# Kernel optimization log

Measured on AMD Instinct MI355X. Metric: run time of the kernel, lower is better.

The kernel has to match this reference:

```python
import jax, jax.numpy as jnp
import numpy as np

B, N, DIM = 32, 1025, 768
H, D = 12, 64
THETA = 100.0


def setup_inputs() -> dict:
    key = jax.random.key(0)
    k0, k1, k2, k3 = jax.random.split(key, 4)
    x = jax.random.normal(k0, (B, N, DIM), dtype=jnp.float32)
    W_qkv = jax.random.normal(k1, (3 * H * D, DIM), dtype=jnp.float32) * 0.02
    W_out = jax.random.normal(k2, (DIM, H * D), dtype=jnp.float32) * 0.02
    b_out = jnp.zeros((DIM,), dtype=jnp.float32)
    # performer random projection buffer: randn(num_features, dim_head) * sqrt(2/dim_head)
    projection = jax.random.normal(k3, (D, D), dtype=jnp.float32) * np.sqrt(2.0 / D)
    # RoPE frequencies for content tokens (n-1 positions, dim_head/2 pairs)
    inv_freq = 1.0 / (THETA ** (np.arange(0, D, 2, dtype=np.float32) / D))  # (D/2,)
    t = np.arange(N - 1, dtype=np.float32)
    angles = np.outer(t, inv_freq)  # (N-1, D/2)
    freqs_cos = jnp.asarray(np.cos(angles), dtype=jnp.float32)
    freqs_sin = jnp.asarray(np.sin(angles), dtype=jnp.float32)
    return {"x": x, "W_qkv": W_qkv, "W_out": W_out, "b_out": b_out,
            "projection": projection, "freqs_cos": freqs_cos, "freqs_sin": freqs_sin}


def reference(x, W_qkv, W_out, b_out, projection, freqs_cos, freqs_sin):
    b, n, _ = x.shape
    h, d = H, D
    # qkv projection and split: 'b n (qkv h d) -> qkv b h n d'
    qkv = jnp.einsum('bnf,gf->bng', x, W_qkv).reshape(b, n, 3, h, d)
    q = jnp.transpose(qkv[:, :, 0], (0, 2, 1, 3))  # (b,h,n,d)
    k = jnp.transpose(qkv[:, :, 1], (0, 2, 1, 3))
    v = jnp.transpose(qkv[:, :, 2], (0, 2, 1, 3))

    def rope(t):
        # rotate content tokens (skip CLS token 0); complex mult as real math
        tc = t[:, :, 1:].reshape(b, h, n - 1, d // 2, 2)
        ev, od = tc[..., 0], tc[..., 1]
        c = freqs_cos[None, None]
        s = freqs_sin[None, None]
        rot = jnp.stack([ev * c - od * s, ev * s + od * c], axis=-1).reshape(b, h, n - 1, d)
        return jnp.concatenate([t[:, :, :1], rot], axis=2)

    q = rope(q)
    k = rope(k)

    def feature_map(t):
        # x * d^{-1/4}, project with (feat, d), relu + eps
        tp = jnp.einsum('bhnd,jd->bhnj', t * (d ** -0.25), projection)
        return jax.nn.relu(tp) + 1e-6

    qf = feature_map(q)
    kf = feature_map(k)

    # non-causal linear attention
    k_sum = kf.sum(axis=-2)                              # (b,h,j)
    context = jnp.einsum('bhnd,bhne->bhde', kf, v)       # (b,h,feat,d)
    D_inv = 1.0 / jnp.einsum('bhnd,bhd->bhn', qf, k_sum)
    out = jnp.einsum('bhde,bhnd,bhn->bhne', context, qf, D_inv)  # (b,h,n,d)

    out = jnp.transpose(out, (0, 2, 1, 3)).reshape(b, n, h * d)
    return jnp.einsum('bnf,gf->bng', out, W_out) + b_out
```

## Files before the change

### kernel.cpp

```cpp
#include <hip/hip_runtime.h>
#include <stdint.h>
#include <stddef.h>

typedef __bf16 bft;
typedef __bf16 bf16x4 __attribute__((ext_vector_type(4)));
typedef __bf16 bf16x8 __attribute__((ext_vector_type(8)));
typedef float f32x4 __attribute__((ext_vector_type(4)));

#define NH 12
#define HD 64
#define SEQ 1025
#define NB 32
#define DMODEL 768
#define MROWS (NB * SEQ)
#define BHN (NB * NH)
#define BSTR 1040
#define MP (NB * BSTR)
#define SEQP 1056

__device__ __forceinline__ void gl_lds16(const void* g, void* l) {
  __builtin_amdgcn_global_load_lds(
      (const __attribute__((address_space(1))) void*)g,
      (__attribute__((address_space(3))) void*)l, 16, 0, 0);
}

__device__ __forceinline__ bf16x4 ds_tr16(const bft* p, int boff) {
  bf16x4 d;
  asm volatile("ds_read_b64_tr_b16 %0, %1 offset:%2"
               : "=v"(d)
               : "v"((const __attribute__((address_space(3))) bft*)p), "i"(boff)
               : "memory");
  return d;
}

__device__ __forceinline__ void lgkm0() {
  asm volatile("s_waitcnt lgkmcnt(0)" ::: "memory");
}

__global__ __launch_bounds__(256) void k_cast(
    const float* __restrict__ S, bft* __restrict__ D, int n4) {
  int i = blockIdx.x * 256 + threadIdx.x;
  if (i < n4) {
    f32x4 v = *(const f32x4*)(S + (size_t)i * 4);
    bf16x4 o;
    o[0] = (bft)v[0]; o[1] = (bft)v[1]; o[2] = (bft)v[2]; o[3] = (bft)v[3];
    *(bf16x4*)(D + (size_t)i * 4) = o;
  }
}

__global__ __launch_bounds__(256) void k_padzero(bft* __restrict__ KFT, bft* __restrict__ VT) {
  int r = blockIdx.x * 256 + threadIdx.x;
  if (r < BHN * 64) {
    bft* a = KFT + (size_t)r * SEQP + 1025;
    bft* b = VT + (size_t)r * SEQP + 1025;
#pragma unroll
    for (int i = 0; i < 31; ++i) { a[i] = (bft)0.f; b[i] = (bft)0.f; }
  }
}

__global__ __launch_bounds__(256) void k_qkv_gemm(
    const bft* __restrict__ X, const bft* __restrict__ W,
    const bft* __restrict__ P,
    const float* __restrict__ FC, const float* __restrict__ FS,
    bft* __restrict__ QF, bft* __restrict__ KFT, bft* __restrict__ VT) {
  __shared__ __align__(16) bft sA[128 * 64];
  __shared__ __align__(16) bft sB[128 * 64];
  __shared__ __align__(16) bft sP[64 * 64];
  const int tid = threadIdx.x;
  const int lane = tid & 63;
  const int lm = lane & 15;
  const int quad = lane >> 4;
  const int wid = tid >> 6;
  const int wm = (wid & 1) << 6;
  const int wn = (wid >> 1) << 6;
  const int m0 = blockIdx.x * 128;
  const int n0 = blockIdx.y * 128;
  const int sw = lm & 7;
  const int o0 = (quad ^ sw) << 3;
  const int o1 = ((4 + quad) ^ sw) << 3;

#pragma unroll
  for (int it = 0; it < 2; it++) {
    int c = it * 256 + tid;
    int row = c >> 3;
    int col = ((c & 7) ^ (row & 7)) << 3;
    gl_lds16(P + row * 64 + col, sP + c * 8);
  }

  f32x4 acc[4][4] = {};

  for (int kt = 0; kt < DMODEL; kt += 64) {
#pragma unroll
    for (int it = 0; it < 4; it++) {
      int c = it * 256 + tid;
      int row = c >> 3;
      int col = ((c & 7) ^ (row & 7)) << 3;
      int ar = m0 + row;
      int b2 = ar / BSTR;
      int nn = ar - b2 * BSTR;
      if (nn > 1024) nn = 1024;
      gl_lds16(X + (size_t)(b2 * SEQ + nn) * DMODEL + kt + col, sA + c * 8);
      gl_lds16(W + (size_t)(n0 + row) * DMODEL + kt + col, sB + c * 8);
    }
    __syncthreads();
#pragma unroll
    for (int kk = 0; kk < 2; kk++) {
      const int off = kk ? o1 : o0;
      bf16x8 af[4], bb[4];
#pragma unroll
      for (int i = 0; i < 4; i++)
        af[i] = *(const bf16x8*)(sA + (wm + i * 16 + lm) * 64 + off);
#pragma unroll
      for (int j = 0; j < 4; j++)
        bb[j] = *(const bf16x8*)(sB + (wn + j * 16 + lm) * 64 + off);
#pragma unroll
      for (int i = 0; i < 4; i++)
#pragma unroll
        for (int j = 0; j < 4; j++)
          acc[i][j] = __builtin_amdgcn_mfma_f32_16x16x32_bf16(af[i], bb[j], acc[i][j], 0, 0, 0);
    }
    __syncthreads();
  }

  const int s = blockIdx.y / 6;
  const int h = ((n0 + wn) - s * DMODEL) >> 6;

  bft* tt = sA + wid * 1024;
  const bft* tl = tt + quad * 128 + lm * 4;

  if (s < 2) {
#pragma unroll
    for (int i = 0; i < 4; i++) {
      const int tbase = m0 + wm + i * 16;
      const int bb2 = tbase / BSTR;
      const int nb = tbase - bb2 * BSTR;
#pragma unroll
      for (int j = 0; j < 4; j++) {
        const int d = j * 16 + lm;
        const int fj = d >> 1;
        bf16x4 w;
#pragma unroll
        for (int r = 0; r < 4; r++) {
          float v = acc[i][j][r];
          float pv = __shfl_xor(v, 1);
          int n = nb + quad * 4 + r;
          float ov = v;
          if (n >= 1) {
            int nc = (n <= 1024) ? n : 1024;
            float cc = FC[(nc - 1) * 32 + fj];
            float ss = FS[(nc - 1) * 32 + fj];
            ov = (d & 1) ? (pv * ss + v * cc) : (v * cc - pv * ss);
          }
          w[r] = (bft)ov;
        }
        *(bf16x4*)(tt + d * 16 + quad * 4) = w;
      }
      lgkm0();
      bf16x4 i0a = ds_tr16(tl, 0);
      bf16x4 i0b = ds_tr16(tl, 128);
      bf16x4 i1a = ds_tr16(tl, 1024);
      bf16x4 i1b = ds_tr16(tl, 1152);
      lgkm0();
      __builtin_amdgcn_sched_barrier(0);
      bf16x8 af0, af1;
#pragma unroll
      for (int e = 0; e < 4; e++) {
        af0[e] = i0a[e]; af0[e + 4] = i0b[e];
        af1[e] = i1a[e]; af1[e + 4] = i1b[e];
      }

      if (s == 0) {
        const int n = nb + lm;
        const bool valid = (n < SEQ);
        bft* dst = QF + ((size_t)(bb2 * NH + h) * SEQ + n) * HD;
#pragma unroll
        for (int j2 = 0; j2 < 4; j2++) {
          bf16x8 p0 = *(const bf16x8*)(sP + (j2 * 16 + lm) * 64 + o0);
          bf16x8 p1 = *(const bf16x8*)(sP + (j2 * 16 + lm) * 64 + o1);
          f32x4 fa = {0.f, 0.f, 0.f, 0.f};
          fa = __builtin_amdgcn_mfma_f32_16x16x32_bf16(p0, af0, fa, 0, 0, 0);
          fa = __builtin_amdgcn_mfma_f32_16x16x32_bf16(p1, af1, fa, 0, 0, 0);
          bf16x4 o;
#pragma unroll
          for (int r = 0; r < 4; r++) {
            float v = fa[r] * 0.35355339f;
            o[r] = (bft)(fmaxf(v, 0.f) + 1e-6f);
          }
          if (valid) *(bf16x4*)(dst + j2 * 16 + quad * 4) = o;
        }
      } else {
        const int nq = nb + quad * 4;
#pragma unroll
        for (int j2 = 0; j2 < 4; j2++) {
          bf16x8 p0 = *(const bf16x8*)(sP + (j2 * 16 + lm) * 64 + o0);
          bf16x8 p1 = *(const bf16x8*)(sP + (j2 * 16 + lm) * 64 + o1);
          f32x4 fa = {0.f, 0.f, 0.f, 0.f};
          fa = __builtin_amdgcn_mfma_f32_16x16x32_bf16(af0, p0, fa, 0, 0, 0);
          fa = __builtin_amdgcn_mfma_f32_16x16x32_bf16(af1, p1, fa, 0, 0, 0);
          bf16x4 o;
#pragma unroll
          for (int r = 0; r < 4; r++) {
            float v = fa[r] * 0.35355339f;
            o[r] = (bft)(fmaxf(v, 0.f) + 1e-6f);
          }
          bft* rowp = KFT + ((size_t)(bb2 * NH + h) * 64 + j2 * 16 + lm) * SEQP;
          if (nq + 3 <= 1024) {
            *(bf16x4*)(rowp + nq) = o;
          } else {
#pragma unroll
            for (int r = 0; r < 4; r++)
              if (nq + r <= 1024) rowp[nq + r] = o[r];
          }
        }
      }
    }
  } else {
#pragma unroll
    for (int i = 0; i < 4; i++) {
      const int tbase = m0 + wm + i * 16;
      const int bb2 = tbase / BSTR;
      const int nb = tbase - bb2 * BSTR;
      const int nq = nb + quad * 4;
#pragma unroll
      for (int j = 0; j < 4; j++) {
        bf16x4 o;
#pragma unroll
        for (int r = 0; r < 4; r++) o[r] = (bft)acc[i][j][r];
        bft* rowp = VT + ((size_t)(bb2 * NH + h) * 64 + j * 16 + lm) * SEQP;
        if (nq + 3 <= 1024) {
          *(bf16x4*)(rowp + nq) = o;
        } else {
#pragma unroll
          for (int r = 0; r < 4; r++)
            if (nq + r <= 1024) rowp[nq + r] = o[r];
        }
      }
    }
  }
}

__global__ __launch_bounds__(256) void k_context(
    const bft* __restrict__ KFT, const bft* __restrict__ VT,
    float* __restrict__ CTX, float* __restrict__ KSUM) {
  __shared__ __align__(16) bft sK[64 * 32];
  __shared__ __align__(16) bft sV[64 * 32];
  const int tid = threadIdx.x;
  const int lane = tid & 63;
  const int lm = lane & 15;
  const int quad = lane >> 4;
  const int wid = tid >> 6;
  const int bh = blockIdx.x;
  const int y = blockIdx.y;
  const int c0 = (33 * y) / 4;
  const int c1 = (33 * (y + 1)) / 4;
  const bft* kb = KFT + (size_t)bh * 64 * SEQP;
  const bft* vb = VT + (size_t)bh * 64 * SEQP;
  const int f0 = wid * 16;
  const int srow = tid >> 2;
  const int sch = (tid & 3) * 8;

  bf16x8 ones;
#pragma unroll
  for (int e = 0; e < 8; e++) ones[e] = (bft)1.0f;

  f32x4 acc[4] = {};
  f32x4 ak = {0.f, 0.f, 0.f, 0.f};

  for (int c = c0; c < c1; ++c) {
    const int t0 = c * 32;
    gl_lds16(kb + (size_t)srow * SEQP + t0 + sch, sK + tid * 8);
    gl_lds16(vb + (size_t)srow * SEQP + t0 + sch, sV + tid * 8);
    __syncthreads();
    bf16x8 a = *(const bf16x8*)(sK + (f0 + lm) * 32 + quad * 8);
    ak = __builtin_amdgcn_mfma_f32_16x16x32_bf16(a, ones, ak, 0, 0, 0);
#pragma unroll
    for (int j = 0; j < 4; j++) {
      bf16x8 b = *(const bf16x8*)(sV + (j * 16 + lm) * 32 + quad * 8);
      acc[j] = __builtin_amdgcn_mfma_f32_16x16x32_bf16(a, b, acc[j], 0, 0, 0);
    }
    __syncthreads();
  }

  float* cp = CTX + (size_t)bh * 4096;
#pragma unroll
  for (int j = 0; j < 4; j++)
#pragma unroll
    for (int r = 0; r < 4; r++)
      atomicAdd(&cp[(f0 + quad * 4 + r) * 64 + j * 16 + lm], acc[j][r]);
  if (lm == 0) {
#pragma unroll
    for (int r = 0; r < 4; r++)
      atomicAdd(&KSUM[bh * 64 + f0 + quad * 4 + r], ak[r]);
  }
}

__global__ __launch_bounds__(256) void k_ctxprep(
    const float* __restrict__ CTX, const float* __restrict__ KSUM,
    bft* __restrict__ CTH, bft* __restrict__ CTL,
    bft* __restrict__ KTH, bft* __restrict__ KTL) {
  const int bh = blockIdx.x;
  const int tid = threadIdx.x;
  const int e = tid >> 2;
  const int g = tid & 3;
  const float* src = CTX + (size_t)bh * 4096 + e;
  bf16x8 h0, l0, h1, l1;
#pragma unroll
  for (int k = 0; k < 16; ++k) {
    float v = src[(g * 16 + k) * 64];
    bft hi = (bft)v;
    bft lo = (bft)(v - (float)hi);
    if (k < 8) { h0[k] = hi; l0[k] = lo; }
    else       { h1[k - 8] = hi; l1[k - 8] = lo; }
  }
  const int c0 = (2 * g) ^ (e & 7);
  const int c1 = (2 * g + 1) ^ (e & 7);
  bft* dh = CTH + (size_t)bh * 4096 + e * 64;
  bft* dl = CTL + (size_t)bh * 4096 + e * 64;
  *(bf16x8*)(dh + c0 * 8) = h0;
  *(bf16x8*)(dh + c1 * 8) = h1;
  *(bf16x8*)(dl + c0 * 8) = l0;
  *(bf16x8*)(dl + c1 * 8) = l1;
  if (tid < 64) {
    float v = KSUM[bh * 64 + tid];
    bft hi = (bft)v;
    KTH[bh * 64 + tid] = hi;
    KTL[bh * 64 + tid] = (bft)(v - (float)hi);
  }
}

__global__ __launch_bounds__(256) void k_qside(
    const bft* __restrict__ QF, const bft* __restrict__ CTH,
    const bft* __restrict__ CTL, const bft* __restrict__ KTH,
    const bft* __restrict__ KTL, bft* __restrict__ ATTN) {
  __shared__ __align__(16) bft sq[128 * 64];
  __shared__ __align__(16) bft sh[64 * 64];
  __shared__ __align__(16) bft sl[64 * 64];
  const int tid = threadIdx.x;
  const int lane = tid & 63;
  const int lm = lane & 15;
  const int quad = lane >> 4;
  const int wid = tid >> 6;
  const int bh = blockIdx.x;
  const int n0 = blockIdx.y * 128;
  const bft* qf = QF + ((size_t)bh * SEQ + n0) * HD;

#pragma unroll
  for (int it = 0; it < 4; it++) {
    int c = it * 256 + tid;
    int row = c >> 3;
    int col = ((c & 7) ^ (row & 7)) << 3;
    gl_lds16(qf + (size_t)row * 64 + col, sq + c * 8);
  }
#pragma unroll
  for (int it = 0; it < 2; it++) {
    int c = it * 256 + tid;
    gl_lds16(CTH + (size_t)bh * 4096 + c * 8, sh + c * 8);
    gl_lds16(CTL + (size_t)bh * 4096 + c * 8, sl + c * 8);
  }
  bf16x8 kh0 = *(const bf16x8*)(KTH + bh * 64 + quad * 8);
  bf16x8 kh1 = *(const bf16x8*)(KTH + bh * 64 + 32 + quad * 8);
  bf16x8 kl0 = *(const bf16x8*)(KTL + bh * 64 + quad * 8);
  bf16x8 kl1 = *(const bf16x8*)(KTL + bh * 64 + 32 + quad * 8);
  bf16x8 zz = {};
  bf16x8 ad0 = (lm == 0) ? kh0 : (lm == 1) ? kl0 : zz;
  bf16x8 ad1 = (lm == 0) ? kh1 : (lm == 1) ? kl1 : zz;
  __syncthreads();

  bf16x8 ah[4][2], al[4][2];
#pragma unroll
  for (int eb = 0; eb < 4; eb++)
#pragma unroll
    for (int kc = 0; kc < 2; kc++) {
      const int off = ((quad + 4 * kc) ^ (lm & 7)) * 8;
      ah[eb][kc] = *(const bf16x8*)(sh + (eb * 16 + lm) * 64 + off);
      al[eb][kc] = *(const bf16x8*)(sl + (eb * 16 + lm) * 64 + off);
    }

  const int b = bh / NH;
  const int h = bh - b * NH;
#pragma unroll
  for (int tb2 = 0; tb2 < 2; tb2++) {
    const int tok0 = (wid * 2 + tb2) * 16;
    const int roff = (tok0 + lm) * 64;
    bf16x8 bq0 = *(const bf16x8*)(sq + roff + ((quad) ^ (lm & 7)) * 8);
    bf16x8 bq1 = *(const bf16x8*)(sq + roff + ((4 + quad) ^ (lm & 7)) * 8);
    f32x4 dacc = {0.f, 0.f, 0.f, 0.f};
    dacc = __builtin_amdgcn_mfma_f32_16x16x32_bf16(ad0, bq0, dacc, 0, 0, 0);
    dacc = __builtin_amdgcn_mfma_f32_16x16x32_bf16(ad1, bq1, dacc, 0, 0, 0);
    const float den = __shfl(dacc[0] + dacc[1], lm);
    const float dinv = 1.0f / den;
    f32x4 fa[4] = {};
#pragma unroll
    for (int eb = 0; eb < 4; eb++) {
      fa[eb] = __builtin_amdgcn_mfma_f32_16x16x32_bf16(ah[eb][0], bq0, fa[eb], 0, 0, 0);
      fa[eb] = __builtin_amdgcn_mfma_f32_16x16x32_bf16(al[eb][0], bq0, fa[eb], 0, 0, 0);
      fa[eb] = __builtin_amdgcn_mfma_f32_16x16x32_bf16(ah[eb][1], bq1, fa[eb], 0, 0, 0);
      fa[eb] = __builtin_amdgcn_mfma_f32_16x16x32_bf16(al[eb][1], bq1, fa[eb], 0, 0, 0);
    }
    const int n = n0 + tok0 + lm;
    if (n < SEQ) {
      bft* dst = ATTN + ((size_t)(b * SEQ + n)) * DMODEL + h * 64;
#pragma unroll
      for (int eb = 0; eb < 4; eb++) {
        bf16x4 o;
#pragma unroll
        for (int r = 0; r < 4; r++) o[r] = (bft)(fa[eb][r] * dinv);
        *(bf16x4*)(dst + eb * 16 + quad * 4) = o;
      }
    }
  }
}

__global__ __launch_bounds__(256) void k_out_gemm(
    const bft* __restrict__ A, const bft* __restrict__ W,
    const float* __restrict__ BIAS, float* __restrict__ OUT) {
  __shared__ __align__(16) bft sA[128 * 64];
  __shared__ __align__(16) bft sB[128 * 64];
  const int tid = threadIdx.x;
  const int lane = tid & 63;
  const int lm = lane & 15;
  const int quad = lane >> 4;
  const int wid = tid >> 6;
  const int wm = (wid & 1) << 6;
  const int wn = (wid >> 1) << 6;
  const int m0 = blockIdx.x * 128;
  const int n0 = blockIdx.y * 128;
  const int sw = lm & 7;
  const int o0 = (quad ^ sw) << 3;
  const int o1 = ((4 + quad) ^ sw) << 3;

  f32x4 acc[4][4] = {};

  for (int kt = 0; kt < DMODEL; kt += 64) {
#pragma unroll
    for (int it = 0; it < 4; it++) {
      int c = it * 256 + tid;
      int row = c >> 3;
      int col = ((c & 7) ^ (row & 7)) << 3;
      int ar = m0 + row;
      if (ar >= MROWS) ar = MROWS - 1;
      gl_lds16(A + (size_t)ar * DMODEL + kt + col, sA + c * 8);
      gl_lds16(W + (size_t)(n0 + row) * DMODEL + kt + col, sB + c * 8);
    }
    __syncthreads();
#pragma unroll
    for (int kk = 0; kk < 2; kk++) {
      const int off = kk ? o1 : o0;
      bf16x8 af[4], bb[4];
#pragma unroll
      for (int i = 0; i < 4; i++)
        af[i] = *(const bf16x8*)(sA + (wm + i * 16 + lm) * 64 + off);
#pragma unroll
      for (int j = 0; j < 4; j++)
        bb[j] = *(const bf16x8*)(sB + (wn + j * 16 + lm) * 64 + off);
#pragma unroll
      for (int i = 0; i < 4; i++)
#pragma unroll
        for (int j = 0; j < 4; j++)
          acc[i][j] = __builtin_amdgcn_mfma_f32_16x16x32_bf16(af[i], bb[j], acc[i][j], 0, 0, 0);
    }
    __syncthreads();
  }

#pragma unroll
  for (int i = 0; i < 4; i++) {
#pragma unroll
    for (int r = 0; r < 4; r++) {
      int m = m0 + wm + i * 16 + quad * 4 + r;
      if (m < MROWS) {
#pragma unroll
        for (int j = 0; j < 4; j++) {
          int g = n0 + wn + j * 16 + lm;
          OUT[(size_t)m * DMODEL + g] = acc[i][j][r] + BIAS[g];
        }
      }
    }
  }
}

extern "C" void kernel_launch(void* const* d_in, const int* in_sizes, int n_in,
                              void* d_out, int out_size, void* d_ws, size_t ws_size,
                              hipStream_t stream) {
  const float* x = (const float*)d_in[0];
  const float* wqkv = (const float*)d_in[1];
  const float* wout = (const float*)d_in[2];
  const float* bout = (const float*)d_in[3];
  const float* proj = (const float*)d_in[4];
  const float* fc = (const float*)d_in[5];
  const float* fs = (const float*)d_in[6];
  float* outp = (float*)d_out;

  char* ws = (char*)d_ws;
  const size_t xb_bytes = (size_t)MROWS * DMODEL * 2;
  const size_t qf_bytes = (size_t)BHN * SEQ * HD * 2;
  const size_t kt_bytes = (size_t)BHN * 64 * SEQP * 2;
  const size_t wqkvb_bytes = (size_t)3 * DMODEL * DMODEL * 2;
  const size_t woutb_bytes = (size_t)DMODEL * DMODEL * 2;
  const size_t ctx_bytes = (size_t)BHN * 64 * 64 * 4;
  const size_t ks_bytes = (size_t)BHN * 64 * 4;
  const size_t ctt_bytes = (size_t)BHN * 64 * 64 * 2;
  const size_t kst_bytes = (size_t)BHN * 64 * 2;

  bft* xb = (bft*)ws;
  bft* qfb = (bft*)(ws + xb_bytes);
  bft* kft = (bft*)(ws + xb_bytes + qf_bytes);
  bft* vt = (bft*)(ws + xb_bytes + qf_bytes + kt_bytes);
  bft* wqkvb = (bft*)(ws + xb_bytes + qf_bytes + 2 * kt_bytes);
  bft* woutb = (bft*)(ws + xb_bytes + qf_bytes + 2 * kt_bytes + wqkvb_bytes);
  bft* projb = (bft*)(ws + xb_bytes + qf_bytes + 2 * kt_bytes + wqkvb_bytes + woutb_bytes);

  float* ctx = (float*)ws;
  float* ksum = (float*)(ws + ctx_bytes);
  bft* cth = (bft*)(ws + ctx_bytes + ks_bytes);
  bft* ctl = (bft*)(ws + ctx_bytes + ks_bytes + ctt_bytes);
  bft* kth = (bft*)(ws + ctx_bytes + ks_bytes + 2 * ctt_bytes);
  bft* ktl = (bft*)(ws + ctx_bytes + ks_bytes + 2 * ctt_bytes + kst_bytes);
  bft* attn = kft;

  dim3 blk(256);
  k_cast<<<dim3((MROWS * DMODEL / 4 + 255) / 256), blk, 0, stream>>>(x, xb, MROWS * DMODEL / 4);
  k_cast<<<dim3((3 * DMODEL * DMODEL / 4 + 255) / 256), blk, 0, stream>>>(wqkv, wqkvb, 3 * DMODEL * DMODEL / 4);
  k_cast<<<dim3((DMODEL * DMODEL / 4 + 255) / 256), blk, 0, stream>>>(wout, woutb, DMODEL * DMODEL / 4);
  k_cast<<<dim3((HD * HD / 4 + 255) / 256), blk, 0, stream>>>(proj, projb, HD * HD / 4);
  k_padzero<<<dim3((BHN * 64 + 255) / 256), blk, 0, stream>>>(kft, vt);

  k_qkv_gemm<<<dim3(MP / 128, 18), blk, 0, stream>>>(xb, wqkvb, projb, fc, fs, qfb, kft, vt);

  hipMemsetAsync(ctx, 0, ctx_bytes + ks_bytes, stream);

  k_context<<<dim3(BHN, 4), blk, 0, stream>>>(kft, vt, ctx, ksum);
  k_ctxprep<<<dim3(BHN), blk, 0, stream>>>(ctx, ksum, cth, ctl, kth, ktl);
  k_qside<<<dim3(BHN, 9), blk, 0, stream>>>(qfb, cth, ctl, kth, ktl, attn);
  k_out_gemm<<<dim3(257, 6), blk, 0, stream>>>(attn, woutb, bout, outp);
  (void)in_sizes; (void)n_in; (void)out_size; (void)ws_size;
}
```

Baseline: 586.3 us.

## Remap GEMM blocks per XCD, precompute padded RoPE tables, vectorize output stores

Both GEMMs now launch on a 1D grid and remap block IDs so each XCD gets a contiguous range of tiles, which should improve L2 reuse of the A and W panels. A small prep kernel builds padded cos/sin tables so the RoPE epilogue can drop its branches and clamping and use a single fma. The per-iteration address math for global-to-LDS loads is hoisted into pointers. The output GEMM swaps its MFMA operands so each lane holds four consecutive columns, letting it write float4 stores with a vector bias load. The cost is an extra tiny launch and workspace for the tables.

```diff
diff --git a/kernel.cpp b/kernel.cpp
--- a/kernel.cpp
+++ b/kernel.cpp
@@ -58,10 +58,27 @@
   }
 }
 
+__global__ __launch_bounds__(256) void k_ropeprep(
+    const float* __restrict__ FC, const float* __restrict__ FS,
+    float* __restrict__ FCP, float* __restrict__ FSP) {
+  int i = blockIdx.x * 256 + threadIdx.x;
+  if (i < 1040 * 32) {
+    int n = i >> 5;
+    int fj = i & 31;
+    float c = 1.f, s = 0.f;
+    if (n >= 1 && n <= 1024) {
+      c = FC[(n - 1) * 32 + fj];
+      s = FS[(n - 1) * 32 + fj];
+    }
+    FCP[i] = c;
+    FSP[i] = s;
+  }
+}
+
 __global__ __launch_bounds__(256) void k_qkv_gemm(
     const bft* __restrict__ X, const bft* __restrict__ W,
     const bft* __restrict__ P,
-    const float* __restrict__ FC, const float* __restrict__ FS,
+    const float* __restrict__ FCP, const float* __restrict__ FSP,
     bft* __restrict__ QF, bft* __restrict__ KFT, bft* __restrict__ VT) {
   __shared__ __align__(16) bft sA[128 * 64];
   __shared__ __align__(16) bft sB[128 * 64];
@@ -73,8 +90,12 @@
   const int wid = tid >> 6;
   const int wm = (wid & 1) << 6;
   const int wn = (wid >> 1) << 6;
-  const int m0 = blockIdx.x * 128;
-  const int n0 = blockIdx.y * 128;
+  const int lin = blockIdx.x;
+  const int logical = (lin & 7) * 585 + (lin >> 3);
+  const int cb = logical % 18;
+  const int rb = logical / 18;
+  const int m0 = rb * 128;
+  const int n0 = cb * 128;
   const int sw = lm & 7;
   const int o0 = (quad ^ sw) << 3;
   const int o1 = ((4 + quad) ^ sw) << 3;
@@ -87,20 +108,31 @@
     gl_lds16(P + row * 64 + col, sP + c * 8);
   }
 
+  const bft* aptr[4];
+  const bft* bptr[4];
+#pragma unroll
+  for (int it = 0; it < 4; it++) {
+    int c = it * 256 + tid;
+    int row = c >> 3;
+    int col = ((c & 7) ^ (row & 7)) << 3;
+    int ar = m0 + row;
+    int b2 = ar / BSTR;
+    int nn = ar - b2 * BSTR;
+    if (nn > 1024) nn = 1024;
+    aptr[it] = X + (size_t)(b2 * SEQ + nn) * DMODEL + col;
+    bptr[it] = W + (size_t)(n0 + row) * DMODEL + col;
+  }
+
   f32x4 acc[4][4] = {};
 
   for (int kt = 0; kt < DMODEL; kt += 64) {
 #pragma unroll
     for (int it = 0; it < 4; it++) {
       int c = it * 256 + tid;
-      int row = c >> 3;
-      int col = ((c & 7) ^ (row & 7)) << 3;
-      int ar = m0 + row;
-      int b2 = ar / BSTR;
-      int nn = ar - b2 * BSTR;
-      if (nn > 1024) nn = 1024;
-      gl_lds16(X + (size_t)(b2 * SEQ + nn) * DMODEL + kt + col, sA + c * 8);
-      gl_lds16(W + (size_t)(n0 + row) * DMODEL + kt + col, sB + c * 8);
+      gl_lds16(aptr[it], sA + c * 8);
+      gl_lds16(bptr[it], sB + c * 8);
+      aptr[it] += 64;
+      bptr[it] += 64;
     }
     __syncthreads();
 #pragma unroll
@@ -122,13 +154,14 @@
     __syncthreads();
   }
 
-  const int s = blockIdx.y / 6;
+  const int s = cb / 6;
   const int h = ((n0 + wn) - s * DMODEL) >> 6;
 
   bft* tt = sA + wid * 1024;
   const bft* tl = tt + quad * 128 + lm * 4;
 
   if (s < 2) {
+    const float sgn = (lm & 1) ? 1.f : -1.f;
 #pragma unroll
     for (int i = 0; i < 4; i++) {
       const int tbase = m0 + wm + i * 16;
@@ -136,22 +169,17 @@
       const int nb = tbase - bb2 * BSTR;
 #pragma unroll
       for (int j = 0; j < 4; j++) {
+        const int fj = (j * 16 + lm) >> 1;
         const int d = j * 16 + lm;
-        const int fj = d >> 1;
         bf16x4 w;
 #pragma unroll
         for (int r = 0; r < 4; r++) {
           float v = acc[i][j][r];
           float pv = __shfl_xor(v, 1);
           int n = nb + quad * 4 + r;
-          float ov = v;
-          if (n >= 1) {
-            int nc = (n <= 1024) ? n : 1024;
-            float cc = FC[(nc - 1) * 32 + fj];
-            float ss = FS[(nc - 1) * 32 + fj];
-            ov = (d & 1) ? (pv * ss + v * cc) : (v * cc - pv * ss);
-          }
-          w[r] = (bft)ov;
+          float cc = FCP[n * 32 + fj];
+          float ss = FSP[n * 32 + fj];
+          w[r] = (bft)fmaf(pv, sgn * ss, v * cc);
         }
         *(bf16x4*)(tt + d * 16 + quad * 4) = w;
       }
@@ -423,24 +451,42 @@
   const int wid = tid >> 6;
   const int wm = (wid & 1) << 6;
   const int wn = (wid >> 1) << 6;
-  const int m0 = blockIdx.x * 128;
-  const int n0 = blockIdx.y * 128;
+  const int lin = blockIdx.x;
+  const int xcd = lin & 7;
+  const int slot = lin >> 3;
+  const int base = (xcd < 6) ? xcd * 193 : 6 * 193 + (xcd - 6) * 192;
+  const int logical = base + slot;
+  const int cb = logical % 6;
+  const int rb = logical / 6;
+  const int m0 = rb * 128;
+  const int n0 = cb * 128;
   const int sw = lm & 7;
   const int o0 = (quad ^ sw) << 3;
   const int o1 = ((4 + quad) ^ sw) << 3;
 
+  const bft* aptr[4];
+  const bft* bptr[4];
+#pragma unroll
+  for (int it = 0; it < 4; it++) {
+    int c = it * 256 + tid;
+    int row = c >> 3;
+    int col = ((c & 7) ^ (row & 7)) << 3;
+    int ar = m0 + row;
+    if (ar >= MROWS) ar = MROWS - 1;
+    aptr[it] = A + (size_t)ar * DMODEL + col;
+    bptr[it] = W + (size_t)(n0 + row) * DMODEL + col;
+  }
+
   f32x4 acc[4][4] = {};
 
   for (int kt = 0; kt < DMODEL; kt += 64) {
 #pragma unroll
     for (int it = 0; it < 4; it++) {
       int c = it * 256 + tid;
-      int row = c >> 3;
-      int col = ((c & 7) ^ (row & 7)) << 3;
-      int ar = m0 + row;
-      if (ar >= MROWS) ar = MROWS - 1;
-      gl_lds16(A + (size_t)ar * DMODEL + kt + col, sA + c * 8);
-      gl_lds16(W + (size_t)(n0 + row) * DMODEL + kt + col, sB + c * 8);
+      gl_lds16(aptr[it], sA + c * 8);
+      gl_lds16(bptr[it], sB + c * 8);
+      aptr[it] += 64;
+      bptr[it] += 64;
     }
     __syncthreads();
 #pragma unroll
@@ -457,22 +503,23 @@
       for (int i = 0; i < 4; i++)
 #pragma unroll
         for (int j = 0; j < 4; j++)
-          acc[i][j] = __builtin_amdgcn_mfma_f32_16x16x32_bf16(af[i], bb[j], acc[i][j], 0, 0, 0);
+          acc[i][j] = __builtin_amdgcn_mfma_f32_16x16x32_bf16(bb[j], af[i], acc[i][j], 0, 0, 0);
     }
     __syncthreads();
   }
 
 #pragma unroll
   for (int i = 0; i < 4; i++) {
-#pragma unroll
-    for (int r = 0; r < 4; r++) {
-      int m = m0 + wm + i * 16 + quad * 4 + r;
-      if (m < MROWS) {
-#pragma unroll
-        for (int j = 0; j < 4; j++) {
-          int g = n0 + wn + j * 16 + lm;
-          OUT[(size_t)m * DMODEL + g] = acc[i][j][r] + BIAS[g];
-        }
+    const int m = m0 + wm + i * 16 + lm;
+    if (m < MROWS) {
+#pragma unroll
+      for (int j = 0; j < 4; j++) {
+        const int g = n0 + wn + j * 16 + quad * 4;
+        f32x4 bias = *(const f32x4*)(BIAS + g);
+        f32x4 o;
+#pragma unroll
+        for (int r = 0; r < 4; r++) o[r] = acc[i][j][r] + bias[r];
+        *(f32x4*)(OUT + (size_t)m * DMODEL + g) = o;
       }
     }
   }
@@ -496,10 +543,12 @@
   const size_t kt_bytes = (size_t)BHN * 64 * SEQP * 2;
   const size_t wqkvb_bytes = (size_t)3 * DMODEL * DMODEL * 2;
   const size_t woutb_bytes = (size_t)DMODEL * DMODEL * 2;
+  const size_t projb_bytes = 8192;
   const size_t ctx_bytes = (size_t)BHN * 64 * 64 * 4;
   const size_t ks_bytes = (size_t)BHN * 64 * 4;
   const size_t ctt_bytes = (size_t)BHN * 64 * 64 * 2;
   const size_t kst_bytes = (size_t)BHN * 64 * 2;
+  const size_t ftab_bytes = (size_t)1040 * 32 * 4;
 
   bft* xb = (bft*)ws;
   bft* qfb = (bft*)(ws + xb_bytes);
@@ -508,6 +557,8 @@
   bft* wqkvb = (bft*)(ws + xb_bytes + qf_bytes + 2 * kt_bytes);
   bft* woutb = (bft*)(ws + xb_bytes + qf_bytes + 2 * kt_bytes + wqkvb_bytes);
   bft* projb = (bft*)(ws + xb_bytes + qf_bytes + 2 * kt_bytes + wqkvb_bytes + woutb_bytes);
+  float* fcp = (float*)(ws + xb_bytes + qf_bytes + 2 * kt_bytes + wqkvb_bytes + woutb_bytes + projb_bytes);
+  float* fsp = (float*)(ws + xb_bytes + qf_bytes + 2 * kt_bytes + wqkvb_bytes + woutb_bytes + projb_bytes + ftab_bytes);
 
   float* ctx = (float*)ws;
   float* ksum = (float*)(ws + ctx_bytes);
@@ -523,14 +574,15 @@
   k_cast<<<dim3((DMODEL * DMODEL / 4 + 255) / 256), blk, 0, stream>>>(wout, woutb, DMODEL * DMODEL / 4);
   k_cast<<<dim3((HD * HD / 4 + 255) / 256), blk, 0, stream>>>(proj, projb, HD * HD / 4);
   k_padzero<<<dim3((BHN * 64 + 255) / 256), blk, 0, stream>>>(kft, vt);
-
-  k_qkv_gemm<<<dim3(MP / 128, 18), blk, 0, stream>>>(xb, wqkvb, projb, fc, fs, qfb, kft, vt);
+  k_ropeprep<<<dim3(130), blk, 0, stream>>>(fc, fs, fcp, fsp);
+
+  k_qkv_gemm<<<dim3(4680), blk, 0, stream>>>(xb, wqkvb, projb, fcp, fsp, qfb, kft, vt);
 
   hipMemsetAsync(ctx, 0, ctx_bytes + ks_bytes, stream);
 
   k_context<<<dim3(BHN, 4), blk, 0, stream>>>(kft, vt, ctx, ksum);
   k_ctxprep<<<dim3(BHN), blk, 0, stream>>>(ctx, ksum, cth, ctl, kth, ktl);
   k_qside<<<dim3(BHN, 9), blk, 0, stream>>>(qfb, cth, ctl, kth, ktl, attn);
-  k_out_gemm<<<dim3(257, 6), blk, 0, stream>>>(attn, woutb, bout, outp);
+  k_out_gemm<<<dim3(1542), blk, 0, stream>>>(attn, woutb, bout, outp);
   (void)in_sizes; (void)n_in; (void)out_size; (void)ws_size;
 }
```

New measurement: 515.9 us. 12.0% less time.
